# Kernel tuning notes

Hardware: AMD Instinct MI355X
Metric: run time of the kernel (lower is better)

The kernel has to match this reference:

```python
import jax, jax.numpy as jnp
import numpy as np

D_MODEL = 1024
N_HEAD = 16
D_K = D_MODEL // N_HEAD
NEG = -1e9


def setup_inputs() -> dict:
    key = jax.random.key(0)
    ks = jax.random.split(key, 9)
    B, S = 2, 2048
    scale = 1.0 / np.sqrt(D_MODEL)
    x = jax.random.normal(ks[0], (B, S, D_MODEL), dtype=jnp.float32)
    mask = jnp.tril(jnp.ones((S, S), dtype=jnp.int32))  # causal: 0 => masked
    Wq = jax.random.normal(ks[1], (D_MODEL, D_MODEL), dtype=jnp.float32) * scale
    bq = jnp.zeros((D_MODEL,), dtype=jnp.float32)
    Wk = jax.random.normal(ks[2], (D_MODEL, D_MODEL), dtype=jnp.float32) * scale
    bk = jnp.zeros((D_MODEL,), dtype=jnp.float32)
    Wv = jax.random.normal(ks[3], (D_MODEL, D_MODEL), dtype=jnp.float32) * scale
    bv = jnp.zeros((D_MODEL,), dtype=jnp.float32)
    Wo = jax.random.normal(ks[4], (D_MODEL, D_MODEL), dtype=jnp.float32) * scale
    bo = jnp.zeros((D_MODEL,), dtype=jnp.float32)
    return {"x": x, "mask": mask, "Wq": Wq, "bq": bq, "Wk": Wk, "bk": bk,
            "Wv": Wv, "bv": bv, "Wo": Wo, "bo": bo}


def reference(x, mask, Wq, bq, Wk, bk, Wv, bv, Wo, bo):
    B, S, _ = x.shape
    # torch Linear: y = x @ W.T + b
    def split_heads(y):  # [B,S,D] -> [B,H,S,d_k]
        return y.reshape(B, S, N_HEAD, D_K).transpose(0, 2, 1, 3)
    Q = split_heads(x @ Wq.T + bq)
    K = split_heads(x @ Wk.T + bk)
    V = split_heads(x @ Wv.T + bv)
    scores = jnp.einsum('bhqd,bhkd->bhqk', Q, K) / jnp.sqrt(jnp.float32(D_K))
    scores = jnp.where(mask[None, None, :, :] == 0, jnp.float32(NEG), scores)
    attn = jax.nn.softmax(scores, axis=-1)
    out = jnp.einsum('bhqk,bhkd->bhqd', attn, V)
    out = out.transpose(0, 2, 1, 3).reshape(B, S, D_MODEL)
    return out @ Wo.T + bo
```

## Files before the change

kernel.cpp:

```cpp
#include <hip/hip_runtime.h>
#include <hip/hip_bf16.h>
#include <stdint.h>

#define DM    1024
#define NHEAD 16
#define DKH   64
#define SEQ   2048
#define NB    2
#define MTOT  (NB*SEQ)
#define LSTR  72

typedef __hip_bfloat16 bf16;
typedef __attribute__((ext_vector_type(8))) short bf16x8;
typedef __attribute__((ext_vector_type(4))) short bf16x4;
typedef __attribute__((ext_vector_type(4))) float f32x4;

#define MFMA16(a,b,c) __builtin_amdgcn_mfma_f32_16x16x32_bf16((a),(b),(c),0,0,0)

__device__ __forceinline__ void async_copy16(const void* g, void* l) {
  __builtin_amdgcn_global_load_lds((const __attribute__((address_space(1))) uint32_t*)g,
                                   (__attribute__((address_space(3))) uint32_t*)l,
                                   16, 0, 0);
}

__device__ __forceinline__ short f32_bf16_bits(float f) {
  uint32_t u = __builtin_bit_cast(uint32_t, f);
  u += 0x7FFFu + ((u >> 16) & 1u);
  return (short)(u >> 16);
}

__global__ __launch_bounds__(256) void k_cvt_all(
    const float* __restrict__ x,  const float* __restrict__ Wq,
    const float* __restrict__ Wk, const float* __restrict__ Wv,
    const float* __restrict__ Wo,
    bf16* __restrict__ xb,  bf16* __restrict__ Wqb, bf16* __restrict__ Wkb,
    bf16* __restrict__ Wvb, bf16* __restrict__ Wob) {
  const int NX = (MTOT*DM)/4;
  const int NW = (DM*DM)/4;
  int i = blockIdx.x * 256 + threadIdx.x;
  const float* s; bf16* d; int j;
  if (i < NX) { s = x; d = xb; j = i; }
  else {
    int t = i - NX;
    int k = t >> 18;
    j = t & (NW - 1);
    s = (k == 0) ? Wq : (k == 1) ? Wk : (k == 2) ? Wv : Wo;
    d = (k == 0) ? Wqb : (k == 1) ? Wkb : (k == 2) ? Wvb : Wob;
  }
  float4 v = ((const float4*)s)[j];
  bf16x4 o;
  o[0] = f32_bf16_bits(v.x);
  o[1] = f32_bf16_bits(v.y);
  o[2] = f32_bf16_bits(v.z);
  o[3] = f32_bf16_bits(v.w);
  ((bf16x4*)d)[j] = o;
}

template <typename OutT>
__device__ __forceinline__ void gemm128_bt(const bf16* __restrict__ A,
                                           const bf16* __restrict__ W,
                                           const float* __restrict__ bias,
                                           OutT* __restrict__ C) {
  __shared__ __align__(16) short As[128*32];
  __shared__ __align__(16) short Bs[128*32];
  const int tid  = threadIdx.x;
  const int lane = tid & 63;
  const int w    = tid >> 6;
  const int wm   = (w & 1) << 6;
  const int wn   = (w >> 1) << 6;
  const int bm   = blockIdx.x << 7;
  const int bn   = blockIdx.y << 7;
  const int m16  = lane & 15;
  const int quad = lane >> 4;
  const int koff = quad << 3;

  const int c0 = (w << 7) | lane;

  f32x4 acc[4][4] = {};

  for (int k0 = 0; k0 < DM; k0 += 32) {
    __syncthreads();
#pragma unroll
    for (int it = 0; it < 2; ++it) {
      int c   = c0 + (it << 6);
      int row = c >> 2;
      int kc  = c & 3;
      async_copy16(A + (size_t)(bm + row) * DM + k0 + (kc << 3),
                   &As[(size_t)((w << 7) + (it << 6)) << 3]);
      async_copy16(W + (size_t)(bn + row) * DM + k0 + (kc << 3),
                   &Bs[(size_t)((w << 7) + (it << 6)) << 3]);
    }
    __syncthreads();

    bf16x8 af[4], bfv[4];
#pragma unroll
    for (int t = 0; t < 4; ++t)
      af[t]  = *(const bf16x8*)&As[(wm + t*16 + m16) * 32 + koff];
#pragma unroll
    for (int t = 0; t < 4; ++t)
      bfv[t] = *(const bf16x8*)&Bs[(wn + t*16 + m16) * 32 + koff];
#pragma unroll
    for (int i = 0; i < 4; ++i)
#pragma unroll
      for (int j = 0; j < 4; ++j)
        acc[i][j] = MFMA16(af[i], bfv[j], acc[i][j]);
  }

  const int crow0 = bm + wm + (quad << 2);
  const int ccol0 = bn + wn + m16;
#pragma unroll
  for (int j = 0; j < 4; ++j) {
    float bv = bias[ccol0 + j*16];
#pragma unroll
    for (int i = 0; i < 4; ++i)
#pragma unroll
      for (int r = 0; r < 4; ++r)
        C[(size_t)(crow0 + i*16 + r) * DM + ccol0 + j*16] =
            (OutT)(acc[i][j][r] + bv);
  }
}

__global__ __launch_bounds__(256) void k_gemm_qkv(
    const bf16* __restrict__ x,
    const bf16* __restrict__ Wq, const bf16* __restrict__ Wk, const bf16* __restrict__ Wv,
    const float* __restrict__ bq, const float* __restrict__ bk, const float* __restrict__ bv,
    bf16* __restrict__ Q, bf16* __restrict__ K, bf16* __restrict__ V) {
  const bf16* W; const float* bias; bf16* C;
  if (blockIdx.z == 0)      { W = Wq; bias = bq; C = Q; }
  else if (blockIdx.z == 1) { W = Wk; bias = bk; C = K; }
  else                      { W = Wv; bias = bv; C = V; }
  gemm128_bt<bf16>(x, W, bias, C);
}

__global__ __launch_bounds__(256) void k_gemm_o(
    const bf16* __restrict__ A, const bf16* __restrict__ W,
    const float* __restrict__ bias, float* __restrict__ C) {
  gemm128_bt<float>(A, W, bias, C);
}

__global__ __launch_bounds__(256) void k_transpose_v(const bf16* __restrict__ V,
                                                     bf16* __restrict__ Vt) {
  __shared__ __align__(16) short tile[64][LSTR];
  const int tid = threadIdx.x;
  const int s0  = blockIdx.x << 6;
  const int bh  = blockIdx.y;
  const int b   = bh >> 4, h = bh & 15;
#pragma unroll
  for (int it = 0; it < 2; ++it) {
    int c = tid + (it << 8);
    int s = c >> 3, dc = c & 7;
    bf16x8 v = *(const bf16x8*)&V[(size_t)(b*SEQ + s0 + s) * DM + h*DKH + (dc << 3)];
    *(bf16x8*)&tile[s][dc << 3] = v;
  }
  __syncthreads();
#pragma unroll
  for (int it = 0; it < 2; ++it) {
    int c = tid + (it << 8);
    int d = c >> 3, sc = c & 7;
    bf16x8 ov;
#pragma unroll
    for (int i = 0; i < 8; ++i) ov[i] = tile[(sc << 3) + i][d];
    *(bf16x8*)&Vt[((size_t)bh * DKH + d) * SEQ + s0 + (sc << 3)] = ov;
  }
}

__global__ __launch_bounds__(256) void k_attn(const bf16* __restrict__ Q,
                                              const bf16* __restrict__ K,
                                              const bf16* __restrict__ Vt,
                                              bf16* __restrict__ ctx) {
  __shared__ __align__(16) short Ks[64*LSTR];
  __shared__ __align__(16) short Vs[64*LSTR];
  __shared__ __align__(16) short PsA[4][16*LSTR];
  __shared__ __align__(16) short PsB[4][16*LSTR];

  const int tid  = threadIdx.x;
  const int lane = tid & 63;
  const int w    = tid >> 6;
  const int pi   = blockIdx.x;
  const int bh   = blockIdx.y;
  const int b    = bh >> 4, h = bh & 15;
  const int qa   = pi, qb = 31 - pi;
  const int m16  = lane & 15, quad = lane >> 4;
  const int koff = quad << 3;

  const int r0 = tid >> 3,         c0 = (tid & 7) << 3;
  const int r1 = (tid + 256) >> 3;

  const bf16* Kb  = K  + (size_t)(b*SEQ) * DM + h*DKH;
  const bf16* Vtb = Vt + (size_t)bh * DKH * SEQ;

  const int qwA = (qa << 6) + (w << 4);
  const int qwB = (qb << 6) + (w << 4);
  const bf16* QbA = Q + (size_t)(b*SEQ + qwA) * DM + h*DKH;
  const bf16* QbB = Q + (size_t)(b*SEQ + qwB) * DM + h*DKH;
  bf16x8 qfA0 = *(const bf16x8*)(QbA + (size_t)m16*DM + koff);
  bf16x8 qfA1 = *(const bf16x8*)(QbA + (size_t)m16*DM + 32 + koff);
  bf16x8 qfB0 = *(const bf16x8*)(QbB + (size_t)m16*DM + koff);
  bf16x8 qfB1 = *(const bf16x8*)(QbB + (size_t)m16*DM + 32 + koff);

  f32x4 oA[4] = {}, oB[4] = {};
  float psA[4] = {0.f,0.f,0.f,0.f}, psB[4] = {0.f,0.f,0.f,0.f};
  short* PwA = PsA[w];
  short* PwB = PsB[w];
  const int qgA = qwA + (quad << 2);
  const int qgB = qwB + (quad << 2);

  bf16x8 pk0 = *(const bf16x8*)(Kb  + (size_t)r0*DM + c0);
  bf16x8 pk1 = *(const bf16x8*)(Kb  + (size_t)r1*DM + c0);
  bf16x8 pv0 = *(const bf16x8*)(Vtb + (size_t)r0*SEQ + c0);
  bf16x8 pv1 = *(const bf16x8*)(Vtb + (size_t)r1*SEQ + c0);

  for (int kt = 0; kt <= qb; ++kt) {
    const int kk0 = kt << 6;
    __syncthreads();
    *(bf16x8*)&Ks[r0*LSTR + c0] = pk0;
    *(bf16x8*)&Ks[r1*LSTR + c0] = pk1;
    *(bf16x8*)&Vs[r0*LSTR + c0] = pv0;
    *(bf16x8*)&Vs[r1*LSTR + c0] = pv1;
    __syncthreads();

    if (kt < qb) {
      const int kn = (kt + 1) << 6;
      pk0 = *(const bf16x8*)(Kb  + (size_t)(kn + r0)*DM + c0);
      pk1 = *(const bf16x8*)(Kb  + (size_t)(kn + r1)*DM + c0);
      pv0 = *(const bf16x8*)(Vtb + (size_t)r0*SEQ + kn + c0);
      pv1 = *(const bf16x8*)(Vtb + (size_t)r1*SEQ + kn + c0);
    }
    const bool doA = (kt <= qa);

    f32x4 scA[4], scB[4];
    if (doA) {
#pragma unroll
      for (int st = 0; st < 4; ++st) {
        bf16x8 kf0 = *(const bf16x8*)&Ks[(st*16 + m16)*LSTR + koff];
        bf16x8 kf1 = *(const bf16x8*)&Ks[(st*16 + m16)*LSTR + 32 + koff];
        f32x4 a = {}; a = MFMA16(qfB0, kf0, a); a = MFMA16(qfB1, kf1, a); scB[st] = a;
        f32x4 c = {}; c = MFMA16(qfA0, kf0, c); c = MFMA16(qfA1, kf1, c); scA[st] = c;
      }
    } else {
#pragma unroll
      for (int st = 0; st < 4; ++st) {
        bf16x8 kf0 = *(const bf16x8*)&Ks[(st*16 + m16)*LSTR + koff];
        bf16x8 kf1 = *(const bf16x8*)&Ks[(st*16 + m16)*LSTR + 32 + koff];
        f32x4 a = {}; a = MFMA16(qfB0, kf0, a); a = MFMA16(qfB1, kf1, a); scB[st] = a;
      }
    }

    if (kt == qb) {
#pragma unroll
      for (int st = 0; st < 4; ++st) {
        int kg = kk0 + st*16 + m16;
#pragma unroll
        for (int r = 0; r < 4; ++r) {
          float e = (kg <= qgB + r) ? __expf(scB[st][r] * 0.125f) : 0.f;
          psB[r] += e;
          PwB[((quad << 2) + r)*LSTR + st*16 + m16] = f32_bf16_bits(e);
        }
      }
    } else {
#pragma unroll
      for (int st = 0; st < 4; ++st)
#pragma unroll
        for (int r = 0; r < 4; ++r) {
          float e = __expf(scB[st][r] * 0.125f);
          psB[r] += e;
          PwB[((quad << 2) + r)*LSTR + st*16 + m16] = f32_bf16_bits(e);
        }
    }
    if (doA) {
      if (kt == qa) {
#pragma unroll
        for (int st = 0; st < 4; ++st) {
          int kg = kk0 + st*16 + m16;
#pragma unroll
          for (int r = 0; r < 4; ++r) {
            float e = (kg <= qgA + r) ? __expf(scA[st][r] * 0.125f) : 0.f;
            psA[r] += e;
            PwA[((quad << 2) + r)*LSTR + st*16 + m16] = f32_bf16_bits(e);
          }
        }
      } else {
#pragma unroll
        for (int st = 0; st < 4; ++st)
#pragma unroll
          for (int r = 0; r < 4; ++r) {
            float e = __expf(scA[st][r] * 0.125f);
            psA[r] += e;
            PwA[((quad << 2) + r)*LSTR + st*16 + m16] = f32_bf16_bits(e);
          }
      }
    }
    asm volatile("s_waitcnt lgkmcnt(0)" ::: "memory");

    if (doA) {
      bf16x8 paB0 = *(const bf16x8*)&PwB[m16*LSTR + koff];
      bf16x8 paB1 = *(const bf16x8*)&PwB[m16*LSTR + 32 + koff];
      bf16x8 paA0 = *(const bf16x8*)&PwA[m16*LSTR + koff];
      bf16x8 paA1 = *(const bf16x8*)&PwA[m16*LSTR + 32 + koff];
#pragma unroll
      for (int t = 0; t < 4; ++t) {
        bf16x8 vf0 = *(const bf16x8*)&Vs[(t*16 + m16)*LSTR + koff];
        bf16x8 vf1 = *(const bf16x8*)&Vs[(t*16 + m16)*LSTR + 32 + koff];
        oB[t] = MFMA16(paB0, vf0, oB[t]);
        oB[t] = MFMA16(paB1, vf1, oB[t]);
        oA[t] = MFMA16(paA0, vf0, oA[t]);
        oA[t] = MFMA16(paA1, vf1, oA[t]);
      }
    } else {
      bf16x8 paB0 = *(const bf16x8*)&PwB[m16*LSTR + koff];
      bf16x8 paB1 = *(const bf16x8*)&PwB[m16*LSTR + 32 + koff];
#pragma unroll
      for (int t = 0; t < 4; ++t) {
        bf16x8 vf0 = *(const bf16x8*)&Vs[(t*16 + m16)*LSTR + koff];
        bf16x8 vf1 = *(const bf16x8*)&Vs[(t*16 + m16)*LSTR + 32 + koff];
        oB[t] = MFMA16(paB0, vf0, oB[t]);
        oB[t] = MFMA16(paB1, vf1, oB[t]);
      }
    }
  }

  bf16* CbA = ctx + (size_t)(b*SEQ + qwA) * DM + h*DKH;
  bf16* CbB = ctx + (size_t)(b*SEQ + qwB) * DM + h*DKH;
#pragma unroll
  for (int r = 0; r < 4; ++r) {
    float va = psA[r], vb = psB[r];
    va += __shfl_xor(va, 1, 64); vb += __shfl_xor(vb, 1, 64);
    va += __shfl_xor(va, 2, 64); vb += __shfl_xor(vb, 2, 64);
    va += __shfl_xor(va, 4, 64); vb += __shfl_xor(vb, 4, 64);
    va += __shfl_xor(va, 8, 64); vb += __shfl_xor(vb, 8, 64);
    float ia = 1.0f / va, ib = 1.0f / vb;
#pragma unroll
    for (int t = 0; t < 4; ++t) {
      CbA[(size_t)((quad << 2) + r) * DM + t*16 + m16] = (bf16)(oA[t][r] * ia);
      CbB[(size_t)((quad << 2) + r) * DM + t*16 + m16] = (bf16)(oB[t][r] * ib);
    }
  }
}

extern "C" void kernel_launch(void* const* d_in, const int* in_sizes, int n_in,
                              void* d_out, int out_size, void* d_ws, size_t ws_size,
                              hipStream_t stream) {
  const float* x  = (const float*)d_in[0];
  const float* Wq = (const float*)d_in[2];
  const float* bq = (const float*)d_in[3];
  const float* Wk = (const float*)d_in[4];
  const float* bk = (const float*)d_in[5];
  const float* Wv = (const float*)d_in[6];
  const float* bv = (const float*)d_in[7];
  const float* Wo = (const float*)d_in[8];
  const float* bo = (const float*)d_in[9];
  float* out = (float*)d_out;

  const size_t SZ = (size_t)MTOT * DM;
  const size_t WZ = (size_t)DM * DM;
  bf16* xb  = (bf16*)d_ws;
  bf16* Wqb = xb  + SZ;
  bf16* Wkb = Wqb + WZ;
  bf16* Wvb = Wkb + WZ;
  bf16* Wob = Wvb + WZ;
  bf16* Qb  = Wob + WZ;
  bf16* Kb  = Qb  + SZ;
  bf16* Vb  = Kb  + SZ;
  bf16* Vtb = Vb  + SZ;
  bf16* Cx  = xb;

  k_cvt_all<<<(SZ/4 + 4*(WZ/4))/256, 256, 0, stream>>>(
      x, Wq, Wk, Wv, Wo, xb, Wqb, Wkb, Wvb, Wob);

  k_gemm_qkv<<<dim3(MTOT/128, DM/128, 3), 256, 0, stream>>>(
      xb, Wqb, Wkb, Wvb, bq, bk, bv, Qb, Kb, Vb);
  k_transpose_v<<<dim3(SEQ/64, NB*NHEAD), 256, 0, stream>>>(Vb, Vtb);
  k_attn<<<dim3(16, NB*NHEAD), 256, 0, stream>>>(Qb, Kb, Vtb, Cx);
  k_gemm_o<<<dim3(MTOT/128, DM/128), 256, 0, stream>>>(Cx, Wob, bo, out);
}
```

Baseline: 223.4 us.

## Split attention KV loop across two blocks and merge partials in combine kernel

```diff
diff --git a/kernel.cpp b/kernel.cpp
--- a/kernel.cpp
+++ b/kernel.cpp
@@ -27,6 +27,10 @@
   uint32_t u = __builtin_bit_cast(uint32_t, f);
   u += 0x7FFFu + ((u >> 16) & 1u);
   return (short)(u >> 16);
+}
+__device__ __forceinline__ float bf16_bits_f32(short s) {
+  uint32_t u = ((uint32_t)(uint16_t)s) << 16;
+  return __builtin_bit_cast(float, u);
 }
 
 __global__ __launch_bounds__(256) void k_cvt_all(
@@ -38,7 +42,7 @@
   const int NX = (MTOT*DM)/4;
   const int NW = (DM*DM)/4;
   int i = blockIdx.x * 256 + threadIdx.x;
-  const float* s; bf16* d; int j;
+  const float* s; bf16* d; int j; float scl = 1.0f;
   if (i < NX) { s = x; d = xb; j = i; }
   else {
     int t = i - NX;
@@ -46,13 +50,14 @@
     j = t & (NW - 1);
     s = (k == 0) ? Wq : (k == 1) ? Wk : (k == 2) ? Wv : Wo;
     d = (k == 0) ? Wqb : (k == 1) ? Wkb : (k == 2) ? Wvb : Wob;
+    if (k == 0) scl = 0.125f;
   }
   float4 v = ((const float4*)s)[j];
   bf16x4 o;
-  o[0] = f32_bf16_bits(v.x);
-  o[1] = f32_bf16_bits(v.y);
-  o[2] = f32_bf16_bits(v.z);
-  o[3] = f32_bf16_bits(v.w);
+  o[0] = f32_bf16_bits(v.x * scl);
+  o[1] = f32_bf16_bits(v.y * scl);
+  o[2] = f32_bf16_bits(v.z * scl);
+  o[3] = f32_bf16_bits(v.w * scl);
   ((bf16x4*)d)[j] = o;
 }
 
@@ -60,6 +65,7 @@
 __device__ __forceinline__ void gemm128_bt(const bf16* __restrict__ A,
                                            const bf16* __restrict__ W,
                                            const float* __restrict__ bias,
+                                           float bscale,
                                            OutT* __restrict__ C) {
   __shared__ __align__(16) short As[128*32];
   __shared__ __align__(16) short Bs[128*32];
@@ -110,7 +116,7 @@
   const int ccol0 = bn + wn + m16;
 #pragma unroll
   for (int j = 0; j < 4; ++j) {
-    float bv = bias[ccol0 + j*16];
+    float bv = bias[ccol0 + j*16] * bscale;
 #pragma unroll
     for (int i = 0; i < 4; ++i)
 #pragma unroll
@@ -125,17 +131,17 @@
     const bf16* __restrict__ Wq, const bf16* __restrict__ Wk, const bf16* __restrict__ Wv,
     const float* __restrict__ bq, const float* __restrict__ bk, const float* __restrict__ bv,
     bf16* __restrict__ Q, bf16* __restrict__ K, bf16* __restrict__ V) {
-  const bf16* W; const float* bias; bf16* C;
-  if (blockIdx.z == 0)      { W = Wq; bias = bq; C = Q; }
-  else if (blockIdx.z == 1) { W = Wk; bias = bk; C = K; }
-  else                      { W = Wv; bias = bv; C = V; }
-  gemm128_bt<bf16>(x, W, bias, C);
+  const bf16* W; const float* bias; bf16* C; float bs;
+  if (blockIdx.z == 0)      { W = Wq; bias = bq; C = Q; bs = 0.125f; }
+  else if (blockIdx.z == 1) { W = Wk; bias = bk; C = K; bs = 1.0f; }
+  else                      { W = Wv; bias = bv; C = V; bs = 1.0f; }
+  gemm128_bt<bf16>(x, W, bias, bs, C);
 }
 
 __global__ __launch_bounds__(256) void k_gemm_o(
     const bf16* __restrict__ A, const bf16* __restrict__ W,
     const float* __restrict__ bias, float* __restrict__ C) {
-  gemm128_bt<float>(A, W, bias, C);
+  gemm128_bt<float>(A, W, bias, 1.0f, C);
 }
 
 __global__ __launch_bounds__(256) void k_transpose_v(const bf16* __restrict__ V,
@@ -167,7 +173,10 @@
 __global__ __launch_bounds__(256) void k_attn(const bf16* __restrict__ Q,
                                               const bf16* __restrict__ K,
                                               const bf16* __restrict__ Vt,
-                                              bf16* __restrict__ ctx) {
+                                              bf16* __restrict__ Po0,
+                                              bf16* __restrict__ Po1,
+                                              float* __restrict__ l0,
+                                              float* __restrict__ l1) {
   __shared__ __align__(16) short Ks[64*LSTR];
   __shared__ __align__(16) short Vs[64*LSTR];
   __shared__ __align__(16) short PsA[4][16*LSTR];
@@ -178,13 +187,16 @@
   const int w    = tid >> 6;
   const int pi   = blockIdx.x;
   const int bh   = blockIdx.y;
+  const int kz   = blockIdx.z;
   const int b    = bh >> 4, h = bh & 15;
   const int qa   = pi, qb = 31 - pi;
   const int m16  = lane & 15, quad = lane >> 4;
   const int koff = quad << 3;
 
-  const int r0 = tid >> 3,         c0 = (tid & 7) << 3;
-  const int r1 = (tid + 256) >> 3;
+  bf16*  Po = kz ? Po1 : Po0;
+  float* lp = kz ? l1  : l0;
+
+  const int r0 = tid >> 3, r1 = (tid + 256) >> 3, c0 = (tid & 7) << 3;
 
   const bf16* Kb  = K  + (size_t)(b*SEQ) * DM + h*DKH;
   const bf16* Vtb = Vt + (size_t)bh * DKH * SEQ;
@@ -205,45 +217,46 @@
   const int qgA = qwA + (quad << 2);
   const int qgB = qwB + (quad << 2);
 
-  bf16x8 pk0 = *(const bf16x8*)(Kb  + (size_t)r0*DM + c0);
-  bf16x8 pk1 = *(const bf16x8*)(Kb  + (size_t)r1*DM + c0);
-  bf16x8 pv0 = *(const bf16x8*)(Vtb + (size_t)r0*SEQ + c0);
-  bf16x8 pv1 = *(const bf16x8*)(Vtb + (size_t)r1*SEQ + c0);
-
-  for (int kt = 0; kt <= qb; ++kt) {
-    const int kk0 = kt << 6;
+  {
+    const int kf = kz << 6;
+    bf16x8 t0 = *(const bf16x8*)(Kb  + (size_t)(kf + r0)*DM + c0);
+    bf16x8 t1 = *(const bf16x8*)(Kb  + (size_t)(kf + r1)*DM + c0);
+    bf16x8 t2 = *(const bf16x8*)(Vtb + (size_t)r0*SEQ + kf + c0);
+    bf16x8 t3 = *(const bf16x8*)(Vtb + (size_t)r1*SEQ + kf + c0);
+    *(bf16x8*)&Ks[r0*LSTR + c0] = t0;
+    *(bf16x8*)&Ks[r1*LSTR + c0] = t1;
+    *(bf16x8*)&Vs[r0*LSTR + c0] = t2;
+    *(bf16x8*)&Vs[r1*LSTR + c0] = t3;
+  }
+
+  bf16x8 pk0, pk1, pv0, pv1;
+  for (int kt = kz; kt <= qb; kt += 2) {
+    if (kt > kz) {
+      __syncthreads();
+      *(bf16x8*)&Ks[r0*LSTR + c0] = pk0;
+      *(bf16x8*)&Ks[r1*LSTR + c0] = pk1;
+      *(bf16x8*)&Vs[r0*LSTR + c0] = pv0;
+      *(bf16x8*)&Vs[r1*LSTR + c0] = pv1;
+    }
     __syncthreads();
-    *(bf16x8*)&Ks[r0*LSTR + c0] = pk0;
-    *(bf16x8*)&Ks[r1*LSTR + c0] = pk1;
-    *(bf16x8*)&Vs[r0*LSTR + c0] = pv0;
-    *(bf16x8*)&Vs[r1*LSTR + c0] = pv1;
-    __syncthreads();
-
-    if (kt < qb) {
-      const int kn = (kt + 1) << 6;
+
+    if (kt + 2 <= qb) {
+      const int kn = (kt + 2) << 6;
       pk0 = *(const bf16x8*)(Kb  + (size_t)(kn + r0)*DM + c0);
       pk1 = *(const bf16x8*)(Kb  + (size_t)(kn + r1)*DM + c0);
       pv0 = *(const bf16x8*)(Vtb + (size_t)r0*SEQ + kn + c0);
       pv1 = *(const bf16x8*)(Vtb + (size_t)r1*SEQ + kn + c0);
     }
     const bool doA = (kt <= qa);
+    const int kk0 = kt << 6;
 
     f32x4 scA[4], scB[4];
-    if (doA) {
-#pragma unroll
-      for (int st = 0; st < 4; ++st) {
-        bf16x8 kf0 = *(const bf16x8*)&Ks[(st*16 + m16)*LSTR + koff];
-        bf16x8 kf1 = *(const bf16x8*)&Ks[(st*16 + m16)*LSTR + 32 + koff];
-        f32x4 a = {}; a = MFMA16(qfB0, kf0, a); a = MFMA16(qfB1, kf1, a); scB[st] = a;
-        f32x4 c = {}; c = MFMA16(qfA0, kf0, c); c = MFMA16(qfA1, kf1, c); scA[st] = c;
-      }
-    } else {
-#pragma unroll
-      for (int st = 0; st < 4; ++st) {
-        bf16x8 kf0 = *(const bf16x8*)&Ks[(st*16 + m16)*LSTR + koff];
-        bf16x8 kf1 = *(const bf16x8*)&Ks[(st*16 + m16)*LSTR + 32 + koff];
-        f32x4 a = {}; a = MFMA16(qfB0, kf0, a); a = MFMA16(qfB1, kf1, a); scB[st] = a;
-      }
+#pragma unroll
+    for (int st = 0; st < 4; ++st) {
+      bf16x8 kf0 = *(const bf16x8*)&Ks[(st*16 + m16)*LSTR + koff];
+      bf16x8 kf1 = *(const bf16x8*)&Ks[(st*16 + m16)*LSTR + 32 + koff];
+      f32x4 a = {}; a = MFMA16(qfB0, kf0, a); a = MFMA16(qfB1, kf1, a); scB[st] = a;
+      if (doA) { f32x4 c = {}; c = MFMA16(qfA0, kf0, c); c = MFMA16(qfA1, kf1, c); scA[st] = c; }
     }
 
     if (kt == qb) {
@@ -252,7 +265,7 @@
         int kg = kk0 + st*16 + m16;
 #pragma unroll
         for (int r = 0; r < 4; ++r) {
-          float e = (kg <= qgB + r) ? __expf(scB[st][r] * 0.125f) : 0.f;
+          float e = (kg <= qgB + r) ? __expf(scB[st][r]) : 0.f;
           psB[r] += e;
           PwB[((quad << 2) + r)*LSTR + st*16 + m16] = f32_bf16_bits(e);
         }
@@ -262,7 +275,7 @@
       for (int st = 0; st < 4; ++st)
 #pragma unroll
         for (int r = 0; r < 4; ++r) {
-          float e = __expf(scB[st][r] * 0.125f);
+          float e = __expf(scB[st][r]);
           psB[r] += e;
           PwB[((quad << 2) + r)*LSTR + st*16 + m16] = f32_bf16_bits(e);
         }
@@ -274,7 +287,7 @@
           int kg = kk0 + st*16 + m16;
 #pragma unroll
           for (int r = 0; r < 4; ++r) {
-            float e = (kg <= qgA + r) ? __expf(scA[st][r] * 0.125f) : 0.f;
+            float e = (kg <= qgA + r) ? __expf(scA[st][r]) : 0.f;
             psA[r] += e;
             PwA[((quad << 2) + r)*LSTR + st*16 + m16] = f32_bf16_bits(e);
           }
@@ -284,7 +297,7 @@
         for (int st = 0; st < 4; ++st)
 #pragma unroll
           for (int r = 0; r < 4; ++r) {
-            float e = __expf(scA[st][r] * 0.125f);
+            float e = __expf(scA[st][r]);
             psA[r] += e;
             PwA[((quad << 2) + r)*LSTR + st*16 + m16] = f32_bf16_bits(e);
           }
@@ -292,9 +305,9 @@
     }
     asm volatile("s_waitcnt lgkmcnt(0)" ::: "memory");
 
+    bf16x8 paB0 = *(const bf16x8*)&PwB[m16*LSTR + koff];
+    bf16x8 paB1 = *(const bf16x8*)&PwB[m16*LSTR + 32 + koff];
     if (doA) {
-      bf16x8 paB0 = *(const bf16x8*)&PwB[m16*LSTR + koff];
-      bf16x8 paB1 = *(const bf16x8*)&PwB[m16*LSTR + 32 + koff];
       bf16x8 paA0 = *(const bf16x8*)&PwA[m16*LSTR + koff];
       bf16x8 paA1 = *(const bf16x8*)&PwA[m16*LSTR + 32 + koff];
 #pragma unroll
@@ -307,8 +320,6 @@
         oA[t] = MFMA16(paA1, vf1, oA[t]);
       }
     } else {
-      bf16x8 paB0 = *(const bf16x8*)&PwB[m16*LSTR + koff];
-      bf16x8 paB1 = *(const bf16x8*)&PwB[m16*LSTR + 32 + koff];
 #pragma unroll
       for (int t = 0; t < 4; ++t) {
         bf16x8 vf0 = *(const bf16x8*)&Vs[(t*16 + m16)*LSTR + koff];
@@ -319,8 +330,8 @@
     }
   }
 
-  bf16* CbA = ctx + (size_t)(b*SEQ + qwA) * DM + h*DKH;
-  bf16* CbB = ctx + (size_t)(b*SEQ + qwB) * DM + h*DKH;
+  bf16* PoA = Po + (size_t)(b*SEQ + qwA) * DM + h*DKH;
+  bf16* PoB = Po + (size_t)(b*SEQ + qwB) * DM + h*DKH;
 #pragma unroll
   for (int r = 0; r < 4; ++r) {
     float va = psA[r], vb = psB[r];
@@ -328,13 +339,34 @@
     va += __shfl_xor(va, 2, 64); vb += __shfl_xor(vb, 2, 64);
     va += __shfl_xor(va, 4, 64); vb += __shfl_xor(vb, 4, 64);
     va += __shfl_xor(va, 8, 64); vb += __shfl_xor(vb, 8, 64);
-    float ia = 1.0f / va, ib = 1.0f / vb;
+    if (m16 == 0) {
+      lp[(size_t)(b*SEQ + qwA + (quad << 2) + r) * NHEAD + h] = va;
+      lp[(size_t)(b*SEQ + qwB + (quad << 2) + r) * NHEAD + h] = vb;
+    }
 #pragma unroll
     for (int t = 0; t < 4; ++t) {
-      CbA[(size_t)((quad << 2) + r) * DM + t*16 + m16] = (bf16)(oA[t][r] * ia);
-      CbB[(size_t)((quad << 2) + r) * DM + t*16 + m16] = (bf16)(oB[t][r] * ib);
-    }
-  }
+      PoA[(size_t)((quad << 2) + r) * DM + t*16 + m16] = (bf16)oA[t][r];
+      PoB[(size_t)((quad << 2) + r) * DM + t*16 + m16] = (bf16)oB[t][r];
+    }
+  }
+}
+
+__global__ __launch_bounds__(256) void k_combine(const bf16* __restrict__ Po0,
+                                                 const bf16* __restrict__ Po1,
+                                                 const float* __restrict__ l0,
+                                                 const float* __restrict__ l1,
+                                                 bf16* __restrict__ ctx) {
+  int i = blockIdx.x * 256 + threadIdx.x;
+  int row = i >> 7;
+  int h   = (i & 127) >> 3;
+  float inv = 1.0f / (l0[(size_t)row * NHEAD + h] + l1[(size_t)row * NHEAD + h]);
+  bf16x8 a = ((const bf16x8*)Po0)[i];
+  bf16x8 bvec = ((const bf16x8*)Po1)[i];
+  bf16x8 o;
+#pragma unroll
+  for (int j = 0; j < 8; ++j)
+    o[j] = f32_bf16_bits((bf16_bits_f32(a[j]) + bf16_bits_f32(bvec[j])) * inv);
+  ((bf16x8*)ctx)[i] = o;
 }
 
 extern "C" void kernel_launch(void* const* d_in, const int* in_sizes, int n_in,
@@ -362,7 +394,12 @@
   bf16* Kb  = Qb  + SZ;
   bf16* Vb  = Kb  + SZ;
   bf16* Vtb = Vb  + SZ;
-  bf16* Cx  = xb;
+
+  bf16*  Po0 = xb;
+  bf16*  Po1 = Vb;
+  float* l0  = (float*)Wqb;
+  float* l1  = l0 + (size_t)MTOT * NHEAD;
+  bf16*  Cx  = Qb;
 
   k_cvt_all<<<(SZ/4 + 4*(WZ/4))/256, 256, 0, stream>>>(
       x, Wq, Wk, Wv, Wo, xb, Wqb, Wkb, Wvb, Wob);
@@ -370,6 +407,7 @@
   k_gemm_qkv<<<dim3(MTOT/128, DM/128, 3), 256, 0, stream>>>(
       xb, Wqb, Wkb, Wvb, bq, bk, bv, Qb, Kb, Vb);
   k_transpose_v<<<dim3(SEQ/64, NB*NHEAD), 256, 0, stream>>>(Vb, Vtb);
-  k_attn<<<dim3(16, NB*NHEAD), 256, 0, stream>>>(Qb, Kb, Vtb, Cx);
+  k_attn<<<dim3(16, NB*NHEAD, 2), 256, 0, stream>>>(Qb, Kb, Vtb, Po0, Po1, l0, l1);
+  k_combine<<<(SZ/8)/256, 256, 0, stream>>>(Po0, Po1, l0, l1, Cx);
   k_gemm_o<<<dim3(MTOT/128, DM/128), 256, 0, stream>>>(Cx, Wob, bo, out);
 }
```

Measured after the change: 224.6 us. About the same (+0.5%).
